# Performance work log

Hardware: AMD Instinct MI355X
Metric: run time of the kernel (lower is better)

Reference implementation:

```python
import jax, jax.numpy as jnp
import numpy as np

B, D, E, C, H = 16384, 4096, 128, 128, 8
DH = E // H  # head_dim = 16


def setup_inputs() -> dict:
    key = jax.random.key(0)
    ks = jax.random.split(key, 15)
    s = 0.02
    return {
        "x": jax.random.normal(ks[0], (B, D), dtype=jnp.float32),
        "label_emb": jax.random.normal(ks[1], (C, E), dtype=jnp.float32) * s,
        "Wf": jax.random.normal(ks[2], (E, D), dtype=jnp.float32) * s,
        "bf": jnp.zeros((E,), dtype=jnp.float32),
        "Wq": jax.random.normal(ks[3], (E, E), dtype=jnp.float32) * s,
        "bq": jnp.zeros((E,), dtype=jnp.float32),
        "Wk": jax.random.normal(ks[4], (E, E), dtype=jnp.float32) * s,
        "bk": jnp.zeros((E,), dtype=jnp.float32),
        "Wv": jax.random.normal(ks[5], (E, E), dtype=jnp.float32) * s,
        "bv": jnp.zeros((E,), dtype=jnp.float32),
        "Wo": jax.random.normal(ks[6], (E, E), dtype=jnp.float32) * s,
        "bo": jnp.zeros((E,), dtype=jnp.float32),
        "Wc": jax.random.normal(ks[7], (C, E), dtype=jnp.float32) * s,
        "bc": jnp.zeros((C,), dtype=jnp.float32),
    }


def reference(x, label_emb, Wf, bf, Wq, bq, Wk, bk, Wv, bv, Wo, bo, Wc, bc):
    # feature projection: [B, D] -> [B, E]  (query token, seq_len = 1)
    f = x @ Wf.T + bf
    # MultiheadAttention in-proj; torch scales q by 1/sqrt(head_dim)
    q = (f @ Wq.T + bq) * (1.0 / jnp.sqrt(jnp.float32(DH)))  # [B, E]
    # keys/values are the same label table for every batch element -> compute once
    k = label_emb @ Wk.T + bk  # [C, E]
    v = label_emb @ Wv.T + bv  # [C, E]
    qh = q.reshape(B, H, DH)
    kh = k.reshape(C, H, DH)
    vh = v.reshape(C, H, DH)
    scores = jnp.einsum('bhd,chd->bhc', qh, kh)  # [B, H, C]
    attn = jax.nn.softmax(scores, axis=-1)
    o = jnp.einsum('bhc,chd->bhd', attn, vh).reshape(B, E)
    o = o @ Wo.T + bo  # out-proj; dropout is identity in eval
    logits = o @ Wc.T + bc  # [B, C]
    return logits
```

## Files before the change

### kernel.cpp

```cpp
#include <hip/hip_runtime.h>
#include <stdint.h>

#define B_N 16384
#define D_N 4096
#define E_N 128
#define C_N 128
#define H_N 8

typedef __attribute__((ext_vector_type(8))) short short8;
typedef __attribute__((ext_vector_type(4))) float f32x4;

__device__ __forceinline__ unsigned short f2bf(float f) {
  union { float f; unsigned u; } c; c.f = f;
  unsigned u = c.u;
  unsigned r = u + 0x7fffu + ((u >> 16) & 1u);
  return (unsigned short)(r >> 16);
}

__device__ __forceinline__ void gload_lds16(const void* g, void* l) {
  __builtin_amdgcn_global_load_lds((const __attribute__((address_space(1))) void*)g,
                                   (__attribute__((address_space(3))) void*)l,
                                   16, 0, 0);
}

__global__ void p1_kernel(
    const float* __restrict__ label_emb, const float* __restrict__ Wk,
    const float* __restrict__ bk, const float* __restrict__ Wv,
    const float* __restrict__ bv, const float* __restrict__ Wf,
    const float* __restrict__ Wc, float* __restrict__ k_ws,
    float* __restrict__ v_ws, unsigned short* __restrict__ Wf_bf,
    unsigned short* __restrict__ Wc_bf) {
  const int NT = gridDim.x * blockDim.x;
  const int t0 = blockIdx.x * blockDim.x + threadIdx.x;
  for (int i = t0; i < C_N * E_N; i += NT) {
    const int c = i >> 7, o = i & 127;
    const float* le = label_emb + c * E_N;
    const float* wk = Wk + o * E_N;
    const float* wv = Wv + o * E_N;
    float ak = 0.f, av = 0.f;
    for (int e = 0; e < E_N; ++e) {
      const float l = le[e];
      ak += l * wk[e];
      av += l * wv[e];
    }
    k_ws[i] = ak + bk[o];
    v_ws[i] = av + bv[o];
  }
  for (int i = t0; i < (E_N * D_N) / 4; i += NT) {
    const f32x4 v4 = ((const f32x4*)Wf)[i];
    unsigned lo = (unsigned)f2bf(v4[0]) | ((unsigned)f2bf(v4[1]) << 16);
    unsigned hi = (unsigned)f2bf(v4[2]) | ((unsigned)f2bf(v4[3]) << 16);
    ((uint2*)Wf_bf)[i] = make_uint2(lo, hi);
  }
  for (int i = t0; i < C_N * E_N; i += NT) Wc_bf[i] = f2bf(Wc[i]);
}

__global__ void p2_kernel(const float* __restrict__ Wq, const float* __restrict__ bq,
                          const float* __restrict__ Wo, const float* __restrict__ k_ws,
                          const float* __restrict__ v_ws, unsigned short* __restrict__ M_bf,
                          unsigned short* __restrict__ V2T_bf, float* __restrict__ bs_ws) {
  const int NT = gridDim.x * blockDim.x;
  const int t0 = blockIdx.x * blockDim.x + threadIdx.x;
  const float scale = 0.25f;
  for (int i = t0; i < 1024 * 128; i += NT) {
    const int hc = i >> 7, e = i & 127;
    const int h = hc >> 7, c = hc & 127;
    float acc = 0.f;
    for (int d = 0; d < 16; ++d)
      acc += Wq[(h * 16 + d) * E_N + e] * k_ws[c * E_N + h * 16 + d];
    M_bf[hc * 128 + e] = f2bf(scale * acc);
  }
  for (int i = t0; i < 128 * 1024; i += NT) {
    const int e2 = i >> 10, hc = i & 1023;
    const int h = hc >> 7, c = hc & 127;
    float acc = 0.f;
    for (int d = 0; d < 16; ++d)
      acc += v_ws[c * E_N + h * 16 + d] * Wo[e2 * E_N + h * 16 + d];
    V2T_bf[e2 * 1024 + hc] = f2bf(acc);
  }
  for (int i = t0; i < 1024; i += NT) {
    const int h = i >> 7, c = i & 127;
    float acc = 0.f;
    for (int d = 0; d < 16; ++d) acc += bq[h * 16 + d] * k_ws[c * E_N + h * 16 + d];
    bs_ws[i] = scale * acc;
  }
}

__global__ __launch_bounds__(256) void g_kernel(
    const float* __restrict__ x, const unsigned short* __restrict__ Wf_bf,
    const float* __restrict__ bfv, unsigned short* __restrict__ f_bf) {
  __shared__ unsigned short Bt[2][128 * 64];
  const int tid = threadIdx.x;
  const int wave = tid >> 6;
  const int lane = tid & 63;
  const int l15 = lane & 15;
  const int kg = lane >> 4;
  const int blk = blockIdx.x;

  const long rowA = (long)blk * 64 + wave * 16 + l15;
  const float* xrow = x + rowA * D_N;

  const f32x4 zero = {0.f, 0.f, 0.f, 0.f};
  f32x4 acc[8];
#pragma unroll
  for (int i = 0; i < 8; ++i) acc[i] = zero;

  f32x4 aC[2][2], aN[2][2];

#pragma unroll
  for (int it = 0; it < 4; ++it) {
    const int slot = it * 256 + tid;
    const int n = slot >> 3, ch = slot & 7;
    gload_lds16(Wf_bf + n * D_N + ((ch ^ (n & 7)) << 3), &Bt[0][slot * 8]);
  }
#pragma unroll
  for (int s = 0; s < 2; ++s) {
    const float* p = xrow + s * 32 + kg * 8;
    aC[s][0] = *(const f32x4*)p;
    aC[s][1] = *(const f32x4*)(p + 4);
    aN[s][0] = aC[s][0];
    aN[s][1] = aC[s][1];
  }
  __syncthreads();

  for (int ks = 0; ks < 64; ++ks) {
    const int buf = ks & 1;
    if (ks + 1 < 64) {
#pragma unroll
      for (int it = 0; it < 4; ++it) {
        const int slot = it * 256 + tid;
        const int n = slot >> 3, ch = slot & 7;
        gload_lds16(Wf_bf + n * D_N + (ks + 1) * 64 + ((ch ^ (n & 7)) << 3),
                    &Bt[buf ^ 1][slot * 8]);
      }
#pragma unroll
      for (int s = 0; s < 2; ++s) {
        const float* p = xrow + (ks + 1) * 64 + s * 32 + kg * 8;
        aN[s][0] = *(const f32x4*)p;
        aN[s][1] = *(const f32x4*)(p + 4);
      }
    }
#pragma unroll
    for (int s = 0; s < 2; ++s) {
      short8 af;
#pragma unroll
      for (int j = 0; j < 4; ++j) {
        af[j] = (short)f2bf(aC[s][0][j]);
        af[4 + j] = (short)f2bf(aC[s][1][j]);
      }
#pragma unroll
      for (int fn = 0; fn < 8; ++fn) {
        const int n = fn * 16 + l15;
        const int g = s * 4 + kg;
        const short8 bq8 = *(const short8*)&Bt[buf][n * 64 + ((g ^ (n & 7)) << 3)];
        acc[fn] = __builtin_amdgcn_mfma_f32_16x16x32_bf16(af, bq8, acc[fn], 0, 0, 0);
      }
    }
    __syncthreads();
#pragma unroll
    for (int s = 0; s < 2; ++s) {
      aC[s][0] = aN[s][0];
      aC[s][1] = aN[s][1];
    }
  }

  const int rbase = blk * 64 + wave * 16;
#pragma unroll
  for (int fn = 0; fn < 8; ++fn) {
    const int col = fn * 16 + l15;
    const float bias = bfv[col];
    const int gran = col >> 3;
#pragma unroll
    for (int r = 0; r < 4; ++r) {
      const int row = rbase + kg * 4 + r;
      f_bf[(long)row * 128 + ((gran ^ (row & 15)) << 3) + (col & 7)] =
          f2bf(acc[fn][r] + bias);
    }
  }
}

__global__ __launch_bounds__(256) void a_kernel(
    const unsigned short* __restrict__ f_bf, const unsigned short* __restrict__ M_bf,
    const float* __restrict__ bs_ws, const unsigned short* __restrict__ V2T_bf,
    const float* __restrict__ bo, const unsigned short* __restrict__ Wc_bf,
    const float* __restrict__ bc, float* __restrict__ out) {
  __shared__ unsigned short fT[64 * 128];
  __shared__ unsigned short pT[64 * 128];
  __shared__ unsigned short oT[64 * 128];
  const int tid = threadIdx.x;
  const int wave = tid >> 6;
  const int lane = tid & 63;
  const int l15 = lane & 15;
  const int kg = lane >> 4;
  const int blk = blockIdx.x;

#pragma unroll
  for (int it = 0; it < 4; ++it) {
    const int slot = it * 256 + tid;
    gload_lds16(f_bf + (long)blk * (64 * 128) + slot * 8, &fT[slot * 8]);
  }
  __syncthreads();

  const int rl = wave * 16 + l15;
  const f32x4 zero = {0.f, 0.f, 0.f, 0.f};
  f32x4 o2[8];
#pragma unroll
  for (int i = 0; i < 8; ++i) o2[i] = zero;

  for (int h = 0; h < 8; ++h) {
    f32x4 sa[8];
#pragma unroll
    for (int i = 0; i < 8; ++i) sa[i] = zero;
#pragma unroll
    for (int s = 0; s < 4; ++s) {
      const short8 af = *(const short8*)&fT[rl * 128 + (((s * 4 + kg) ^ l15) << 3)];
#pragma unroll
      for (int fn = 0; fn < 8; ++fn) {
        const int hc = h * 128 + fn * 16 + l15;
        const short8 bq8 = *(const short8*)(M_bf + (long)hc * 128 + s * 32 + kg * 8);
        sa[fn] = __builtin_amdgcn_mfma_f32_16x16x32_bf16(af, bq8, sa[fn], 0, 0, 0);
      }
    }
#pragma unroll
    for (int fn = 0; fn < 8; ++fn) {
      const float b = bs_ws[h * 128 + fn * 16 + l15];
#pragma unroll
      for (int r = 0; r < 4; ++r) sa[fn][r] += b;
    }
    float pv[8][4];
#pragma unroll
    for (int r = 0; r < 4; ++r) {
      float m = sa[0][r];
#pragma unroll
      for (int fn = 1; fn < 8; ++fn) m = fmaxf(m, sa[fn][r]);
      m = fmaxf(m, __shfl_xor(m, 1));
      m = fmaxf(m, __shfl_xor(m, 2));
      m = fmaxf(m, __shfl_xor(m, 4));
      m = fmaxf(m, __shfl_xor(m, 8));
      float sum = 0.f;
      float ev[8];
#pragma unroll
      for (int fn = 0; fn < 8; ++fn) {
        ev[fn] = __expf(sa[fn][r] - m);
        sum += ev[fn];
      }
      sum += __shfl_xor(sum, 1);
      sum += __shfl_xor(sum, 2);
      sum += __shfl_xor(sum, 4);
      sum += __shfl_xor(sum, 8);
      const float inv = 1.f / sum;
#pragma unroll
      for (int fn = 0; fn < 8; ++fn) pv[fn][r] = ev[fn] * inv;
    }
#pragma unroll
    for (int fn = 0; fn < 8; ++fn) {
      const int col = fn * 16 + l15;
      const int gran = col >> 3;
#pragma unroll
      for (int r = 0; r < 4; ++r) {
        const int row = wave * 16 + kg * 4 + r;
        pT[row * 128 + ((gran ^ (row & 15)) << 3) + (col & 7)] = f2bf(pv[fn][r]);
      }
    }
    __syncthreads();
#pragma unroll
    for (int s = 0; s < 4; ++s) {
      const short8 af = *(const short8*)&pT[rl * 128 + (((s * 4 + kg) ^ l15) << 3)];
#pragma unroll
      for (int fn = 0; fn < 8; ++fn) {
        const int e2 = fn * 16 + l15;
        const short8 bq8 =
            *(const short8*)(V2T_bf + (long)e2 * 1024 + h * 128 + s * 32 + kg * 8);
        o2[fn] = __builtin_amdgcn_mfma_f32_16x16x32_bf16(af, bq8, o2[fn], 0, 0, 0);
      }
    }
    __syncthreads();
  }

#pragma unroll
  for (int fn = 0; fn < 8; ++fn) {
    const int col = fn * 16 + l15;
    const float b = bo[col];
    const int gran = col >> 3;
#pragma unroll
    for (int r = 0; r < 4; ++r) {
      const int row = wave * 16 + kg * 4 + r;
      oT[row * 128 + ((gran ^ (row & 15)) << 3) + (col & 7)] = f2bf(o2[fn][r] + b);
    }
  }
  __syncthreads();

  f32x4 la[8];
#pragma unroll
  for (int i = 0; i < 8; ++i) la[i] = zero;
#pragma unroll
  for (int s = 0; s < 4; ++s) {
    const short8 af = *(const short8*)&oT[rl * 128 + (((s * 4 + kg) ^ l15) << 3)];
#pragma unroll
    for (int fn = 0; fn < 8; ++fn) {
      const short8 bq8 = *(const short8*)(Wc_bf + (fn * 16 + l15) * 128 + s * 32 + kg * 8);
      la[fn] = __builtin_amdgcn_mfma_f32_16x16x32_bf16(af, bq8, la[fn], 0, 0, 0);
    }
  }
#pragma unroll
  for (int fn = 0; fn < 8; ++fn) {
    const int col = fn * 16 + l15;
    const float b = bc[col];
#pragma unroll
    for (int r = 0; r < 4; ++r) {
      const long row = (long)blk * 64 + wave * 16 + kg * 4 + r;
      out[row * 128 + col] = la[fn][r] + b;
    }
  }
}

extern "C" void kernel_launch(void* const* d_in, const int* in_sizes, int n_in,
                              void* d_out, int out_size, void* d_ws, size_t ws_size,
                              hipStream_t stream) {
  (void)in_sizes; (void)n_in; (void)out_size; (void)ws_size;
  const float* x   = (const float*)d_in[0];
  const float* le  = (const float*)d_in[1];
  const float* Wf  = (const float*)d_in[2];
  const float* bf  = (const float*)d_in[3];
  const float* Wq  = (const float*)d_in[4];
  const float* bq  = (const float*)d_in[5];
  const float* Wk  = (const float*)d_in[6];
  const float* bk  = (const float*)d_in[7];
  const float* Wv  = (const float*)d_in[8];
  const float* bv  = (const float*)d_in[9];
  const float* Wo  = (const float*)d_in[10];
  const float* bo  = (const float*)d_in[11];
  const float* Wc  = (const float*)d_in[12];
  const float* bc  = (const float*)d_in[13];
  float* out = (float*)d_out;

  char* ws = (char*)d_ws;
  unsigned short* Wf_bf  = (unsigned short*)(ws + 0);
  unsigned short* f_bf   = (unsigned short*)(ws + 1048576);
  unsigned short* M_bf   = (unsigned short*)(ws + 5242880);
  unsigned short* V2T_bf = (unsigned short*)(ws + 5505024);
  unsigned short* Wc_bf  = (unsigned short*)(ws + 5767168);
  float* k_ws            = (float*)(ws + 5799936);
  float* v_ws            = (float*)(ws + 5865472);
  float* bs_ws           = (float*)(ws + 5931008);

  hipLaunchKernelGGL(p1_kernel, dim3(256), dim3(256), 0, stream,
                     le, Wk, bk, Wv, bv, Wf, Wc, k_ws, v_ws, Wf_bf, Wc_bf);
  hipLaunchKernelGGL(p2_kernel, dim3(256), dim3(256), 0, stream,
                     Wq, bq, Wo, k_ws, v_ws, M_bf, V2T_bf, bs_ws);
  hipLaunchKernelGGL(g_kernel, dim3(B_N / 64), dim3(256), 0, stream,
                     x, Wf_bf, bf, f_bf);
  hipLaunchKernelGGL(a_kernel, dim3(B_N / 64), dim3(256), 0, stream,
                     f_bf, M_bf, bs_ws, V2T_bf, bo, Wc_bf, bc, out);
}
```

Baseline: 607.1 us.

## Merge prep kernels, split heads across wave groups, stage weights in LDS

Fuses the two preprocessing kernels into a single block-specialised kernel that computes per-head K/V in shared memory, removing one launch and the k/v workspace round trip. The feature GEMM now uses 512-thread blocks with two wave groups, each covering half of the output columns. The attention kernel splits the heads between two wave groups and stages M, V2T and Wc tiles in swizzled LDS instead of reading them from global memory, then sums the partial outputs through shared memory. This adds LDS pressure and extra synchronisation, and leaves half the waves idle during the final classifier GEMM.

```diff
diff --git a/kernel.cpp b/kernel.cpp
--- a/kernel.cpp
+++ b/kernel.cpp
@@ -1,20 +1,13 @@
 #include <hip/hip_runtime.h>
 #include <stdint.h>
 
-#define B_N 16384
-#define D_N 4096
-#define E_N 128
-#define C_N 128
-#define H_N 8
-
 typedef __attribute__((ext_vector_type(8))) short short8;
 typedef __attribute__((ext_vector_type(4))) float f32x4;
 
-__device__ __forceinline__ unsigned short f2bf(float f) {
+__device__ __forceinline__ unsigned f2bf(float f) {
   union { float f; unsigned u; } c; c.f = f;
   unsigned u = c.u;
-  unsigned r = u + 0x7fffu + ((u >> 16) & 1u);
-  return (unsigned short)(r >> 16);
+  return (u + 0x7fffu + ((u >> 16) & 1u)) >> 16;
 }
 
 __device__ __forceinline__ void gload_lds16(const void* g, void* l) {
@@ -23,119 +16,140 @@
                                    16, 0, 0);
 }
 
-__global__ void p1_kernel(
+__device__ __forceinline__ void stage32k(const unsigned short* __restrict__ src,
+                                         int stride, unsigned short* dst, int hgtid) {
+#pragma unroll
+  for (int it = 0; it < 8; ++it) {
+    const int slot = it * 256 + hgtid;
+    const int n = slot >> 4, ch = slot & 15;
+    gload_lds16(src + n * stride + ((ch ^ (n & 15)) << 3), dst + slot * 8);
+  }
+}
+
+__global__ __launch_bounds__(256) void p_kernel(
     const float* __restrict__ label_emb, const float* __restrict__ Wk,
     const float* __restrict__ bk, const float* __restrict__ Wv,
-    const float* __restrict__ bv, const float* __restrict__ Wf,
-    const float* __restrict__ Wc, float* __restrict__ k_ws,
-    float* __restrict__ v_ws, unsigned short* __restrict__ Wf_bf,
-    unsigned short* __restrict__ Wc_bf) {
-  const int NT = gridDim.x * blockDim.x;
-  const int t0 = blockIdx.x * blockDim.x + threadIdx.x;
-  for (int i = t0; i < C_N * E_N; i += NT) {
-    const int c = i >> 7, o = i & 127;
-    const float* le = label_emb + c * E_N;
-    const float* wk = Wk + o * E_N;
-    const float* wv = Wv + o * E_N;
-    float ak = 0.f, av = 0.f;
-    for (int e = 0; e < E_N; ++e) {
-      const float l = le[e];
-      ak += l * wk[e];
-      av += l * wv[e];
-    }
-    k_ws[i] = ak + bk[o];
-    v_ws[i] = av + bv[o];
-  }
-  for (int i = t0; i < (E_N * D_N) / 4; i += NT) {
-    const f32x4 v4 = ((const f32x4*)Wf)[i];
-    unsigned lo = (unsigned)f2bf(v4[0]) | ((unsigned)f2bf(v4[1]) << 16);
-    unsigned hi = (unsigned)f2bf(v4[2]) | ((unsigned)f2bf(v4[3]) << 16);
-    ((uint2*)Wf_bf)[i] = make_uint2(lo, hi);
-  }
-  for (int i = t0; i < C_N * E_N; i += NT) Wc_bf[i] = f2bf(Wc[i]);
-}
-
-__global__ void p2_kernel(const float* __restrict__ Wq, const float* __restrict__ bq,
-                          const float* __restrict__ Wo, const float* __restrict__ k_ws,
-                          const float* __restrict__ v_ws, unsigned short* __restrict__ M_bf,
-                          unsigned short* __restrict__ V2T_bf, float* __restrict__ bs_ws) {
-  const int NT = gridDim.x * blockDim.x;
-  const int t0 = blockIdx.x * blockDim.x + threadIdx.x;
-  const float scale = 0.25f;
-  for (int i = t0; i < 1024 * 128; i += NT) {
-    const int hc = i >> 7, e = i & 127;
-    const int h = hc >> 7, c = hc & 127;
-    float acc = 0.f;
-    for (int d = 0; d < 16; ++d)
-      acc += Wq[(h * 16 + d) * E_N + e] * k_ws[c * E_N + h * 16 + d];
-    M_bf[hc * 128 + e] = f2bf(scale * acc);
-  }
-  for (int i = t0; i < 128 * 1024; i += NT) {
-    const int e2 = i >> 10, hc = i & 1023;
-    const int h = hc >> 7, c = hc & 127;
-    float acc = 0.f;
-    for (int d = 0; d < 16; ++d)
-      acc += v_ws[c * E_N + h * 16 + d] * Wo[e2 * E_N + h * 16 + d];
-    V2T_bf[e2 * 1024 + hc] = f2bf(acc);
-  }
-  for (int i = t0; i < 1024; i += NT) {
-    const int h = i >> 7, c = i & 127;
-    float acc = 0.f;
-    for (int d = 0; d < 16; ++d) acc += bq[h * 16 + d] * k_ws[c * E_N + h * 16 + d];
-    bs_ws[i] = scale * acc;
-  }
-}
-
-__global__ __launch_bounds__(256) void g_kernel(
+    const float* __restrict__ bv, const float* __restrict__ Wq,
+    const float* __restrict__ bq, const float* __restrict__ Wo,
+    const float* __restrict__ Wf, const float* __restrict__ Wc,
+    unsigned short* __restrict__ M_bf, unsigned short* __restrict__ V2T_bf,
+    unsigned short* __restrict__ Wc_bf, unsigned short* __restrict__ Wf_bf,
+    float* __restrict__ bs_ws) {
+  __shared__ float leS[128 * 128];
+  __shared__ float KhS[128 * 16];
+  __shared__ float VhS[128 * 16];
+  const int blk = blockIdx.x;
+  const int tid = threadIdx.x;
+
+  if (blk < 8) {
+    const int h16 = blk * 16;
+    for (int i = tid; i < 4096; i += 256)
+      ((f32x4*)leS)[i] = ((const f32x4*)label_emb)[i];
+    __syncthreads();
+    for (int o = tid; o < 2048; o += 256) {
+      const int c = o >> 4, d = o & 15;
+      const float* lrow = leS + c * 128;
+      const float* wkr = Wk + (h16 + d) * 128;
+      const float* wvr = Wv + (h16 + d) * 128;
+      float ak = 0.f, av = 0.f;
+      for (int e = 0; e < 128; ++e) {
+        const float l = lrow[e];
+        ak += l * wkr[e];
+        av += l * wvr[e];
+      }
+      KhS[o] = ak + bk[h16 + d];
+      VhS[o] = av + bv[h16 + d];
+    }
+    __syncthreads();
+    for (int o = tid; o < 16384; o += 256) {
+      const int c = o >> 7, e = o & 127;
+      const float* kc = KhS + c * 16;
+      float acc = 0.f;
+#pragma unroll
+      for (int d = 0; d < 16; ++d) acc += Wq[(h16 + d) * 128 + e] * kc[d];
+      M_bf[(blk * 128 + c) * 128 + e] = (unsigned short)f2bf(0.25f * acc);
+    }
+    for (int o = tid; o < 16384; o += 256) {
+      const int e2 = o >> 7, c = o & 127;
+      const float* vc = VhS + c * 16;
+      float acc = 0.f;
+#pragma unroll
+      for (int d = 0; d < 16; ++d) acc += Wo[e2 * 128 + h16 + d] * vc[d];
+      V2T_bf[e2 * 1024 + blk * 128 + c] = (unsigned short)f2bf(acc);
+    }
+    for (int c = tid; c < 128; c += 256) {
+      const float* kc = KhS + c * 16;
+      float acc = 0.f;
+#pragma unroll
+      for (int d = 0; d < 16; ++d) acc += bq[h16 + d] * kc[d];
+      bs_ws[blk * 128 + c] = 0.25f * acc;
+    }
+  } else if (blk < 72) {
+    const int base = (blk - 8) * 2048;
+#pragma unroll
+    for (int i = 0; i < 8; ++i) {
+      const int idx = base + i * 256 + tid;
+      const f32x4 v4 = ((const f32x4*)Wf)[idx];
+      const unsigned lo = f2bf(v4[0]) | (f2bf(v4[1]) << 16);
+      const unsigned hi = f2bf(v4[2]) | (f2bf(v4[3]) << 16);
+      ((uint2*)Wf_bf)[idx] = make_uint2(lo, hi);
+    }
+  } else {
+    for (int i = tid; i < 4096; i += 256) {
+      const f32x4 v4 = ((const f32x4*)Wc)[i];
+      const unsigned lo = f2bf(v4[0]) | (f2bf(v4[1]) << 16);
+      const unsigned hi = f2bf(v4[2]) | (f2bf(v4[3]) << 16);
+      ((uint2*)Wc_bf)[i] = make_uint2(lo, hi);
+    }
+  }
+}
+
+__global__ __launch_bounds__(512) void g_kernel(
     const float* __restrict__ x, const unsigned short* __restrict__ Wf_bf,
     const float* __restrict__ bfv, unsigned short* __restrict__ f_bf) {
-  __shared__ unsigned short Bt[2][128 * 64];
+  __shared__ unsigned short Bt[2][8192];
   const int tid = threadIdx.x;
-  const int wave = tid >> 6;
-  const int lane = tid & 63;
-  const int l15 = lane & 15;
-  const int kg = lane >> 4;
+  const int wave = tid >> 6, lane = tid & 63;
+  const int l15 = lane & 15, kg = lane >> 4;
+  const int r = wave & 3, cg = wave >> 2;
   const int blk = blockIdx.x;
-
-  const long rowA = (long)blk * 64 + wave * 16 + l15;
-  const float* xrow = x + rowA * D_N;
+  const long rowA = (long)blk * 64 + r * 16 + l15;
+  const float* xrow = x + rowA * 4096;
 
   const f32x4 zero = {0.f, 0.f, 0.f, 0.f};
-  f32x4 acc[8];
-#pragma unroll
-  for (int i = 0; i < 8; ++i) acc[i] = zero;
-
+  f32x4 acc[4];
+#pragma unroll
+  for (int i = 0; i < 4; ++i) acc[i] = zero;
   f32x4 aC[2][2], aN[2][2];
 
 #pragma unroll
-  for (int it = 0; it < 4; ++it) {
-    const int slot = it * 256 + tid;
+  for (int it = 0; it < 2; ++it) {
+    const int slot = it * 512 + tid;
     const int n = slot >> 3, ch = slot & 7;
-    gload_lds16(Wf_bf + n * D_N + ((ch ^ (n & 7)) << 3), &Bt[0][slot * 8]);
+    gload_lds16(Wf_bf + n * 4096 + ((ch ^ (n & 7)) << 3), &Bt[0][slot * 8]);
   }
 #pragma unroll
   for (int s = 0; s < 2; ++s) {
     const float* p = xrow + s * 32 + kg * 8;
     aC[s][0] = *(const f32x4*)p;
     aC[s][1] = *(const f32x4*)(p + 4);
-    aN[s][0] = aC[s][0];
-    aN[s][1] = aC[s][1];
   }
   __syncthreads();
 
   for (int ks = 0; ks < 64; ++ks) {
     const int buf = ks & 1;
-    if (ks + 1 < 64) {
-#pragma unroll
-      for (int it = 0; it < 4; ++it) {
-        const int slot = it * 256 + tid;
+    if (ks < 63) {
+      const int k0 = (ks + 1) * 64;
+#pragma unroll
+      for (int it = 0; it < 2; ++it) {
+        const int slot = it * 512 + tid;
         const int n = slot >> 3, ch = slot & 7;
-        gload_lds16(Wf_bf + n * D_N + (ks + 1) * 64 + ((ch ^ (n & 7)) << 3),
+        gload_lds16(Wf_bf + n * 4096 + k0 + ((ch ^ (n & 7)) << 3),
                     &Bt[buf ^ 1][slot * 8]);
       }
 #pragma unroll
       for (int s = 0; s < 2; ++s) {
-        const float* p = xrow + (ks + 1) * 64 + s * 32 + kg * 8;
+        const float* p = xrow + k0 + s * 32 + kg * 8;
         aN[s][0] = *(const f32x4*)p;
         aN[s][1] = *(const f32x4*)(p + 4);
       }
@@ -144,95 +158,102 @@
     for (int s = 0; s < 2; ++s) {
       short8 af;
 #pragma unroll
-      for (int j = 0; j < 4; ++j) {
-        af[j] = (short)f2bf(aC[s][0][j]);
-        af[4 + j] = (short)f2bf(aC[s][1][j]);
-      }
-#pragma unroll
-      for (int fn = 0; fn < 8; ++fn) {
-        const int n = fn * 16 + l15;
+      for (int q = 0; q < 4; ++q) {
+        af[q] = (short)f2bf(aC[s][0][q]);
+        af[4 + q] = (short)f2bf(aC[s][1][q]);
+      }
+#pragma unroll
+      for (int fn = 0; fn < 4; ++fn) {
+        const int n = cg * 64 + fn * 16 + l15;
         const int g = s * 4 + kg;
-        const short8 bq8 = *(const short8*)&Bt[buf][n * 64 + ((g ^ (n & 7)) << 3)];
-        acc[fn] = __builtin_amdgcn_mfma_f32_16x16x32_bf16(af, bq8, acc[fn], 0, 0, 0);
+        const short8 b8 = *(const short8*)&Bt[buf][n * 64 + ((g ^ (n & 7)) << 3)];
+        acc[fn] = __builtin_amdgcn_mfma_f32_16x16x32_bf16(af, b8, acc[fn], 0, 0, 0);
       }
     }
     __syncthreads();
-#pragma unroll
-    for (int s = 0; s < 2; ++s) {
-      aC[s][0] = aN[s][0];
-      aC[s][1] = aN[s][1];
-    }
-  }
-
-  const int rbase = blk * 64 + wave * 16;
-#pragma unroll
-  for (int fn = 0; fn < 8; ++fn) {
-    const int col = fn * 16 + l15;
+    if (ks < 63) {
+#pragma unroll
+      for (int s = 0; s < 2; ++s) {
+        aC[s][0] = aN[s][0];
+        aC[s][1] = aN[s][1];
+      }
+    }
+  }
+
+#pragma unroll
+  for (int fn = 0; fn < 4; ++fn) {
+    const int col = cg * 64 + fn * 16 + l15;
     const float bias = bfv[col];
     const int gran = col >> 3;
 #pragma unroll
-    for (int r = 0; r < 4; ++r) {
-      const int row = rbase + kg * 4 + r;
-      f_bf[(long)row * 128 + ((gran ^ (row & 15)) << 3) + (col & 7)] =
-          f2bf(acc[fn][r] + bias);
-    }
-  }
-}
-
-__global__ __launch_bounds__(256) void a_kernel(
+    for (int rr = 0; rr < 4; ++rr) {
+      const int rowloc = r * 16 + kg * 4 + rr;
+      const long grow = (long)blk * 64 + rowloc;
+      f_bf[grow * 128 + ((gran ^ (rowloc & 15)) << 3) + (col & 7)] =
+          (unsigned short)f2bf(acc[fn][rr] + bias);
+    }
+  }
+}
+
+__global__ __launch_bounds__(512) void a_kernel(
     const unsigned short* __restrict__ f_bf, const unsigned short* __restrict__ M_bf,
     const float* __restrict__ bs_ws, const unsigned short* __restrict__ V2T_bf,
     const float* __restrict__ bo, const unsigned short* __restrict__ Wc_bf,
     const float* __restrict__ bc, float* __restrict__ out) {
-  __shared__ unsigned short fT[64 * 128];
-  __shared__ unsigned short pT[64 * 128];
-  __shared__ unsigned short oT[64 * 128];
+  __shared__ unsigned short stg[2][16384];
+  __shared__ unsigned short pT[2][8192];
   const int tid = threadIdx.x;
-  const int wave = tid >> 6;
-  const int lane = tid & 63;
-  const int l15 = lane & 15;
-  const int kg = lane >> 4;
+  const int wave = tid >> 6, lane = tid & 63;
+  const int l15 = lane & 15, kg = lane >> 4;
+  const int r = wave & 3, j = wave >> 2;
+  const int hgtid = tid & 255;
   const int blk = blockIdx.x;
-
-#pragma unroll
-  for (int it = 0; it < 4; ++it) {
-    const int slot = it * 256 + tid;
-    gload_lds16(f_bf + (long)blk * (64 * 128) + slot * 8, &fT[slot * 8]);
-  }
-  __syncthreads();
-
-  const int rl = wave * 16 + l15;
+  const int rl = r * 16 + l15;
+  const long grow = (long)blk * 64 + rl;
+
+  short8 fa[4];
+#pragma unroll
+  for (int s = 0; s < 4; ++s)
+    fa[s] = *(const short8*)(f_bf + grow * 128 + (((s * 4 + kg) ^ (rl & 15)) << 3));
+
   const f32x4 zero = {0.f, 0.f, 0.f, 0.f};
   f32x4 o2[8];
 #pragma unroll
   for (int i = 0; i < 8; ++i) o2[i] = zero;
 
-  for (int h = 0; h < 8; ++h) {
+  unsigned short* stj = stg[j];
+  stage32k(M_bf + (j * 4) * 128 * 128, 128, stj, hgtid);
+  __syncthreads();
+
+  for (int hh = 0; hh < 4; ++hh) {
+    const int h = j * 4 + hh;
     f32x4 sa[8];
 #pragma unroll
     for (int i = 0; i < 8; ++i) sa[i] = zero;
 #pragma unroll
     for (int s = 0; s < 4; ++s) {
-      const short8 af = *(const short8*)&fT[rl * 128 + (((s * 4 + kg) ^ l15) << 3)];
 #pragma unroll
       for (int fn = 0; fn < 8; ++fn) {
-        const int hc = h * 128 + fn * 16 + l15;
-        const short8 bq8 = *(const short8*)(M_bf + (long)hc * 128 + s * 32 + kg * 8);
-        sa[fn] = __builtin_amdgcn_mfma_f32_16x16x32_bf16(af, bq8, sa[fn], 0, 0, 0);
-      }
-    }
+        const int n = fn * 16 + l15;
+        const short8 b8 = *(const short8*)&stj[n * 128 + (((s * 4 + kg) ^ (n & 15)) << 3)];
+        sa[fn] = __builtin_amdgcn_mfma_f32_16x16x32_bf16(fa[s], b8, sa[fn], 0, 0, 0);
+      }
+    }
+    asm volatile("s_waitcnt lgkmcnt(0)" ::: "memory");
+    stage32k(V2T_bf + h * 128, 1024, stj, hgtid);
+
 #pragma unroll
     for (int fn = 0; fn < 8; ++fn) {
       const float b = bs_ws[h * 128 + fn * 16 + l15];
 #pragma unroll
-      for (int r = 0; r < 4; ++r) sa[fn][r] += b;
+      for (int rr = 0; rr < 4; ++rr) sa[fn][rr] += b;
     }
     float pv[8][4];
 #pragma unroll
-    for (int r = 0; r < 4; ++r) {
-      float m = sa[0][r];
-#pragma unroll
-      for (int fn = 1; fn < 8; ++fn) m = fmaxf(m, sa[fn][r]);
+    for (int rr = 0; rr < 4; ++rr) {
+      float m = sa[0][rr];
+#pragma unroll
+      for (int fn = 1; fn < 8; ++fn) m = fmaxf(m, sa[fn][rr]);
       m = fmaxf(m, __shfl_xor(m, 1));
       m = fmaxf(m, __shfl_xor(m, 2));
       m = fmaxf(m, __shfl_xor(m, 4));
@@ -241,7 +262,7 @@
       float ev[8];
 #pragma unroll
       for (int fn = 0; fn < 8; ++fn) {
-        ev[fn] = __expf(sa[fn][r] - m);
+        ev[fn] = __expf(sa[fn][rr] - m);
         sum += ev[fn];
       }
       sum += __shfl_xor(sum, 1);
@@ -250,66 +271,94 @@
       sum += __shfl_xor(sum, 8);
       const float inv = 1.f / sum;
 #pragma unroll
-      for (int fn = 0; fn < 8; ++fn) pv[fn][r] = ev[fn] * inv;
+      for (int fn = 0; fn < 8; ++fn) pv[fn][rr] = ev[fn] * inv;
     }
 #pragma unroll
     for (int fn = 0; fn < 8; ++fn) {
       const int col = fn * 16 + l15;
       const int gran = col >> 3;
 #pragma unroll
-      for (int r = 0; r < 4; ++r) {
-        const int row = wave * 16 + kg * 4 + r;
-        pT[row * 128 + ((gran ^ (row & 15)) << 3) + (col & 7)] = f2bf(pv[fn][r]);
-      }
-    }
+      for (int rr = 0; rr < 4; ++rr) {
+        const int rowloc = r * 16 + kg * 4 + rr;
+        pT[j][rowloc * 128 + ((gran ^ (rowloc & 15)) << 3) + (col & 7)] =
+            (unsigned short)f2bf(pv[fn][rr]);
+      }
+    }
+    short8 pa[4];
+#pragma unroll
+    for (int s = 0; s < 4; ++s)
+      pa[s] = *(const short8*)&pT[j][rl * 128 + (((s * 4 + kg) ^ (rl & 15)) << 3)];
     __syncthreads();
+
 #pragma unroll
     for (int s = 0; s < 4; ++s) {
-      const short8 af = *(const short8*)&pT[rl * 128 + (((s * 4 + kg) ^ l15) << 3)];
 #pragma unroll
       for (int fn = 0; fn < 8; ++fn) {
-        const int e2 = fn * 16 + l15;
-        const short8 bq8 =
-            *(const short8*)(V2T_bf + (long)e2 * 1024 + h * 128 + s * 32 + kg * 8);
-        o2[fn] = __builtin_amdgcn_mfma_f32_16x16x32_bf16(af, bq8, o2[fn], 0, 0, 0);
-      }
+        const int n = fn * 16 + l15;
+        const short8 b8 = *(const short8*)&stj[n * 128 + (((s * 4 + kg) ^ (n & 15)) << 3)];
+        o2[fn] = __builtin_amdgcn_mfma_f32_16x16x32_bf16(pa[s], b8, o2[fn], 0, 0, 0);
+      }
+    }
+    asm volatile("s_waitcnt lgkmcnt(0)" ::: "memory");
+    if (hh < 3) {
+      stage32k(M_bf + (h + 1) * 128 * 128, 128, stj, hgtid);
+    } else if (j == 0) {
+      stage32k(Wc_bf, 128, stg[0], hgtid);
     }
     __syncthreads();
   }
 
-#pragma unroll
-  for (int fn = 0; fn < 8; ++fn) {
-    const int col = fn * 16 + l15;
-    const float b = bo[col];
-    const int gran = col >> 3;
-#pragma unroll
-    for (int r = 0; r < 4; ++r) {
-      const int row = wave * 16 + kg * 4 + r;
-      oT[row * 128 + ((gran ^ (row & 15)) << 3) + (col & 7)] = f2bf(o2[fn][r] + b);
+  if (j == 1) {
+    float* o2x = (float*)stg[1];
+#pragma unroll
+    for (int fn = 0; fn < 8; ++fn) {
+      const int col = fn * 16 + l15;
+#pragma unroll
+      for (int rr = 0; rr < 4; ++rr)
+        o2x[(r * 16 + kg * 4 + rr) * 128 + col] = o2[fn][rr];
     }
   }
   __syncthreads();
-
-  f32x4 la[8];
-#pragma unroll
-  for (int i = 0; i < 8; ++i) la[i] = zero;
-#pragma unroll
-  for (int s = 0; s < 4; ++s) {
-    const short8 af = *(const short8*)&oT[rl * 128 + (((s * 4 + kg) ^ l15) << 3)];
+  if (j == 0) {
+    const float* o2x = (const float*)stg[1];
 #pragma unroll
     for (int fn = 0; fn < 8; ++fn) {
-      const short8 bq8 = *(const short8*)(Wc_bf + (fn * 16 + l15) * 128 + s * 32 + kg * 8);
-      la[fn] = __builtin_amdgcn_mfma_f32_16x16x32_bf16(af, bq8, la[fn], 0, 0, 0);
-    }
-  }
-#pragma unroll
-  for (int fn = 0; fn < 8; ++fn) {
-    const int col = fn * 16 + l15;
-    const float b = bc[col];
-#pragma unroll
-    for (int r = 0; r < 4; ++r) {
-      const long row = (long)blk * 64 + wave * 16 + kg * 4 + r;
-      out[row * 128 + col] = la[fn][r] + b;
+      const int col = fn * 16 + l15;
+      const float bov = bo[col];
+      const int gran = col >> 3;
+#pragma unroll
+      for (int rr = 0; rr < 4; ++rr) {
+        const int rowloc = r * 16 + kg * 4 + rr;
+        const float v = o2[fn][rr] + o2x[rowloc * 128 + col] + bov;
+        pT[0][rowloc * 128 + ((gran ^ (rowloc & 15)) << 3) + (col & 7)] =
+            (unsigned short)f2bf(v);
+      }
+    }
+    short8 oa[4];
+#pragma unroll
+    for (int s = 0; s < 4; ++s)
+      oa[s] = *(const short8*)&pT[0][rl * 128 + (((s * 4 + kg) ^ (rl & 15)) << 3)];
+    f32x4 la[8];
+#pragma unroll
+    for (int i = 0; i < 8; ++i) la[i] = zero;
+#pragma unroll
+    for (int s = 0; s < 4; ++s) {
+#pragma unroll
+      for (int fn = 0; fn < 8; ++fn) {
+        const int n = fn * 16 + l15;
+        const short8 b8 = *(const short8*)&stg[0][n * 128 + (((s * 4 + kg) ^ (n & 15)) << 3)];
+        la[fn] = __builtin_amdgcn_mfma_f32_16x16x32_bf16(oa[s], b8, la[fn], 0, 0, 0);
+      }
+    }
+#pragma unroll
+    for (int fn = 0; fn < 8; ++fn) {
+      const int col = fn * 16 + l15;
+      const float bcv = bc[col];
+#pragma unroll
+      for (int rr = 0; rr < 4; ++rr) {
+        const int rowloc = r * 16 + kg * 4 + rr;
+        out[((long)blk * 64 + rowloc) * 128 + col] = la[fn][rr] + bcv;
+      }
     }
   }
 }
@@ -340,16 +389,13 @@
   unsigned short* M_bf   = (unsigned short*)(ws + 5242880);
   unsigned short* V2T_bf = (unsigned short*)(ws + 5505024);
   unsigned short* Wc_bf  = (unsigned short*)(ws + 5767168);
-  float* k_ws            = (float*)(ws + 5799936);
-  float* v_ws            = (float*)(ws + 5865472);
-  float* bs_ws           = (float*)(ws + 5931008);
-
-  hipLaunchKernelGGL(p1_kernel, dim3(256), dim3(256), 0, stream,
-                     le, Wk, bk, Wv, bv, Wf, Wc, k_ws, v_ws, Wf_bf, Wc_bf);
-  hipLaunchKernelGGL(p2_kernel, dim3(256), dim3(256), 0, stream,
-                     Wq, bq, Wo, k_ws, v_ws, M_bf, V2T_bf, bs_ws);
-  hipLaunchKernelGGL(g_kernel, dim3(B_N / 64), dim3(256), 0, stream,
+  float* bs_ws           = (float*)(ws + 5799936);
+
+  hipLaunchKernelGGL(p_kernel, dim3(73), dim3(256), 0, stream,
+                     le, Wk, bk, Wv, bv, Wq, bq, Wo, Wf, Wc,
+                     M_bf, V2T_bf, Wc_bf, Wf_bf, bs_ws);
+  hipLaunchKernelGGL(g_kernel, dim3(256), dim3(512), 0, stream,
                      x, Wf_bf, bf, f_bf);
-  hipLaunchKernelGGL(a_kernel, dim3(B_N / 64), dim3(256), 0, stream,
+  hipLaunchKernelGGL(a_kernel, dim3(256), dim3(512), 0, stream,
                      f_bf, M_bf, bs_ws, V2T_bf, bo, Wc_bf, bc, out);
 }
```

Measured after the change: 538.9 us. 1.13x faster.
